# Kernel optimization log

Hardware: AMD Instinct MI355X
Metric: run time of the kernel (lower is better)

Reference implementation:

```python
import jax, jax.numpy as jnp
import numpy as np

N = 4096
F_IN = 128
N_HEADS = 4
N_HIDDEN = 16  # out_features 64 // 4 heads
LRELU_SLOPE = 0.2


def setup_inputs() -> dict:
    key = jax.random.key(0)
    k1, k2, k3 = jax.random.split(key, 3)
    x = jax.random.normal(k1, (N, F_IN), dtype=jnp.float32)
    adj = jax.random.randint(jax.random.fold_in(key, 7), (N, N), 0, 2, dtype=jnp.int32)
    # linearinput weight: in_features -> n_heads * n_hidden (no bias)
    W = jax.random.normal(k2, (F_IN, N_HEADS * N_HIDDEN), dtype=jnp.float32) / np.sqrt(F_IN)
    # attn weight: 2*n_hidden -> 1 (no bias), shared across heads
    attn_w = jax.random.normal(k3, (2 * N_HIDDEN,), dtype=jnp.float32) / np.sqrt(2 * N_HIDDEN)
    return {"x": x, "adj": adj, "W": W, "attn_w": attn_w}


def reference(x, adj, W, attn_w):
    n = x.shape[0]
    # h: (N, H, Dh)
    h = (x @ W).reshape(n, N_HEADS, N_HIDDEN)
    # attn is linear on [h_i || h_j] => e_ij = lrelu(src_i + dst_j)
    a_src = attn_w[:N_HIDDEN]
    a_dst = attn_w[N_HIDDEN:]
    src = jnp.einsum('nhd,d->nh', h, a_src)  # (N, H)
    dst = jnp.einsum('nhd,d->nh', h, a_dst)  # (N, H)
    e = jax.nn.leaky_relu(src[:, None, :] + dst[None, :, :], negative_slope=LRELU_SLOPE)  # (N, N, H)
    a = jax.nn.softmax(e, axis=1)  # softmax over neighbor axis j
    # dropout in eval mode: identity
    attn_res = jnp.einsum('ijh,jhf->ihf', a, h)  # (N, H, Dh)
    return attn_res.reshape(n, N_HEADS * N_HIDDEN)  # is_concat=True
```

## Files before the change

kernel.cpp:

```cpp
#include <hip/hip_runtime.h>

#define NN 4096
#define FIN 128
#define NHEAD 4
#define NHID 16
#define NCOL 64
#define SLOPE 0.2f
#define CHUNK 64
#define NCH 64
#define NCOLS 17
#define RPAD 20

__device__ __forceinline__ float lrelu(float v){ return v > 0.f ? v : SLOPE * v; }

__device__ __forceinline__ unsigned fkey(float f){
  unsigned b = __float_as_uint(f);
  return b ^ ((b & 0x80000000u) ? 0xFFFFFFFFu : 0x80000000u);
}
__device__ __forceinline__ float fkey_inv(unsigned k){
  unsigned b = (k & 0x80000000u) ? (k ^ 0x80000000u) : ~k;
  return __uint_as_float(b);
}

__global__ __launch_bounds__(256) void gemm_h_k(const float* __restrict__ x,
                                                const float* __restrict__ W,
                                                const float* __restrict__ aw,
                                                float* __restrict__ h,
                                                float* __restrict__ src,
                                                float* __restrict__ dst){
  __shared__ __align__(16) float wl[FIN][NCOL];
  __shared__ float xlT[FIN][10];
  __shared__ float hs[8][NCOL + 1];
  int t = threadIdx.x;
  int row0 = blockIdx.x * 8;
  for (int k4 = t; k4 < FIN * NCOL / 4; k4 += 256)
    ((float4*)&wl[0][0])[k4] = ((const float4*)W)[k4];
  for (int k = t; k < 8 * FIN; k += 256){
    int r = k >> 7, d = k & 127;
    xlT[d][r] = x[(row0 + r) * FIN + d];
  }
  __syncthreads();
  int col = t & 63, rb = t >> 6;
  float a0 = 0.f, a1 = 0.f;
  #pragma unroll
  for (int d = 0; d < FIN; ++d){
    float wv = wl[d][col];
    float2 xv = *(const float2*)&xlT[d][rb * 2];
    a0 = fmaf(xv.x, wv, a0);
    a1 = fmaf(xv.y, wv, a1);
  }
  h[(row0 + rb * 2) * NCOL + col] = a0;     hs[rb * 2][col] = a0;
  h[(row0 + rb * 2 + 1) * NCOL + col] = a1; hs[rb * 2 + 1][col] = a1;
  __syncthreads();
  if (t < 32){
    int r = t >> 2, hd = t & 3;
    float s = 0.f, d = 0.f;
    #pragma unroll
    for (int f = 0; f < NHID; ++f){
      float v = hs[r][hd * NHID + f];
      s = fmaf(v, aw[f], s);
      d = fmaf(v, aw[NHID + f], d);
    }
    src[hd * NN + row0 + r] = s;
    dst[hd * NN + row0 + r] = d;
  }
}

__global__ __launch_bounds__(512) void ranksc_k(const float* __restrict__ dst,
                                                unsigned long long* __restrict__ ksort,
                                                unsigned* __restrict__ dkey){
  int ib = blockIdx.x;
  int hd = blockIdx.y;
  __shared__ __align__(16) unsigned long long keys2[64][66];
  __shared__ int wsum[8][64];
  int t = threadIdx.x;
  const float* dp = dst + hd * NN;
  for (int j = t; j < NN; j += 512)
    keys2[j >> 6][j & 63] = ((unsigned long long)fkey(dp[j]) << 32) | (unsigned)j;
  __syncthreads();
  int g = t >> 3, c = t & 7;
  unsigned long long mk[8];
  #pragma unroll
  for (int r = 0; r < 8; ++r) mk[r] = keys2[ib][c * 8 + r];
  int cnt[8] = {0, 0, 0, 0, 0, 0, 0, 0};
  const ulonglong2* kp = (const ulonglong2*)&keys2[g][0];
  #pragma unroll 4
  for (int q = 0; q < 32; ++q){
    ulonglong2 kk = kp[q];
    #pragma unroll
    for (int r = 0; r < 8; ++r){
      cnt[r] += (kk.x < mk[r]) ? 1 : 0;
      cnt[r] += (kk.y < mk[r]) ? 1 : 0;
    }
  }
  #pragma unroll
  for (int r = 0; r < 8; ++r){
    cnt[r] += __shfl_down(cnt[r], 32);
    cnt[r] += __shfl_down(cnt[r], 16);
    cnt[r] += __shfl_down(cnt[r], 8);
  }
  int w = t >> 6;
  if ((t & 63) < 8){
    #pragma unroll
    for (int r = 0; r < 8; ++r) wsum[w][c * 8 + r] = cnt[r];
  }
  __syncthreads();
  if (t < 64){
    int rank = 0;
    #pragma unroll
    for (int w2 = 0; w2 < 8; ++w2) rank += wsum[w2][t];
    unsigned long long key = keys2[ib][t];
    ksort[hd * NN + rank] = key;
    dkey[hd * NN + rank]  = (unsigned)(key >> 32);
  }
}

__global__ __launch_bounds__(256) void scanA_k(const float* __restrict__ h,
                                               const unsigned long long* __restrict__ ksort,
                                               float* __restrict__ PL2,
                                               float* __restrict__ SL2,
                                               float* __restrict__ ctP,
                                               float* __restrict__ ctS){
  int ch = blockIdx.x;
  int hd = blockIdx.y;
  int t = threadIdx.x;
  int base = ch * CHUNK;
  __shared__ float e02[CHUNK], e1[CHUNK];
  __shared__ int   pms[CHUNK];
  __shared__ float hl[CHUNK][RPAD];
  __shared__ float PLs[CHUNK][RPAD], SLs[CHUNK][RPAD];
  if (t < CHUNK){
    unsigned long long key = ksort[hd * NN + base + t];
    float d = fkey_inv((unsigned)(key >> 32));
    e02[t] = __expf(0.2f * d);
    e1[t]  = __expf(d);
    pms[t] = (int)(unsigned)key;
    hl[t][16] = 1.0f;
  }
  __syncthreads();
  {
    int col = t & 15, r0 = t >> 4;
    #pragma unroll
    for (int it = 0; it < 4; ++it){
      int r = it * 16 + r0;
      hl[r][col] = h[pms[r] * NCOL + hd * NHID + col];
    }
  }
  __syncthreads();
  if (t < NCOLS){
    int col = t;
    float run = 0.f;
    #pragma unroll
    for (int r = 0; r < CHUNK; ++r){
      PLs[r][col] = run;
      run = fmaf(e02[r], hl[r][col], run);
    }
    ctP[ch * 68 + hd * 17 + col] = run;
  } else if (t >= 64 && t < 64 + NCOLS){
    int col = t - 64;
    float rs = 0.f;
    #pragma unroll
    for (int r = CHUNK - 1; r >= 0; --r){
      rs = fmaf(e1[r], hl[r][col], rs);
      SLs[r][col] = rs;
    }
    ctS[ch * 68 + hd * 17 + col] = rs;
  }
  __syncthreads();
  #pragma unroll
  for (int n = 0; n < 5; ++n){
    int idx = n * 256 + t;
    int r = idx / RPAD, c = idx % RPAD;
    PL2[(hd * NN + base + r) * RPAD + c] = PLs[r][c];
    SL2[(hd * NN + base + r) * RPAD + c] = SLs[r][c];
  }
}

__global__ __launch_bounds__(256) void out_k(const float* __restrict__ src,
                                             const unsigned* __restrict__ dkey,
                                             const float* __restrict__ PL2,
                                             const float* __restrict__ SL2,
                                             const float* __restrict__ ctP,
                                             const float* __restrict__ ctS,
                                             float* __restrict__ out){
  __shared__ __align__(16) unsigned dk[NN];
  __shared__ __align__(16) float oP[NCH + 1][68];
  __shared__ __align__(16) float oS[NCH][68];
  int t = threadIdx.x;
  int hd = blockIdx.x & 3, ig = blockIdx.x >> 2;
  const unsigned* dkp = dkey + hd * NN;
  #pragma unroll
  for (int n = 0; n < 4; ++n)
    ((uint4*)dk)[n * 256 + t] = ((const uint4*)dkp)[n * 256 + t];
  #pragma unroll
  for (int n = 0; n < 5; ++n){
    int idx = n * 256 + t;
    if (idx < 1088){
      ((float4*)&oP[0][0])[idx] = ((const float4*)ctP)[idx];
      ((float4*)&oS[0][0])[idx] = ((const float4*)ctS)[idx];
    }
  }
  __syncthreads();
  if (t < 68){
    float run = 0.f;
    #pragma unroll
    for (int c = 0; c < NCH; ++c){ float v = oP[c][t]; oP[c][t] = run; run += v; }
    oP[NCH][t] = run;
  } else if (t >= 128 && t < 196){
    int cc = t - 128;
    float rs = 0.f;
    #pragma unroll
    for (int c = NCH - 1; c >= 0; --c){ float v = oS[c][cc]; oS[c][cc] = rs; rs += v; }
  }
  __syncthreads();
  int p = t >> 2, q = t & 3;
  int i = ig * 64 + p;
  float s = src[hd * NN + i];
  unsigned tu = fkey(-s);
  int lo = 0, hi = NN;
  while (lo < hi){
    int mid = (lo + hi) >> 1;
    if (dk[mid] < tu) lo = mid + 1; else hi = mid;
  }
  int k = lo;
  float4 res;
  if (k == NN){
    float inv = 1.0f / oP[NCH][hd * 17 + 16];
    res.x = oP[NCH][hd * 17 + q * 4 + 0] * inv;
    res.y = oP[NCH][hd * 17 + q * 4 + 1] * inv;
    res.z = oP[NCH][hd * 17 + q * 4 + 2] * inv;
    res.w = oP[NCH][hd * 17 + q * 4 + 3] * inv;
  } else {
    float dmax = fkey_inv(dk[NN - 1]);
    float m = lrelu(s + dmax);
    float alpha = __expf(0.2f * s - m);
    float beta  = __expf(s - m);
    int ch = k >> 6;
    const float* P2 = PL2 + (size_t)(hd * NN + k) * RPAD;
    const float* S2 = SL2 + (size_t)(hd * NN + k) * RPAD;
    float4 p4 = *(const float4*)(P2 + q * 4);
    float4 s4 = *(const float4*)(S2 + q * 4);
    float den = alpha * (P2[16] + oP[ch][hd * 17 + 16])
              + beta  * (S2[16] + oS[ch][hd * 17 + 16]);
    float inv = 1.0f / den;
    res.x = (alpha * (p4.x + oP[ch][hd * 17 + q * 4 + 0])
           + beta  * (s4.x + oS[ch][hd * 17 + q * 4 + 0])) * inv;
    res.y = (alpha * (p4.y + oP[ch][hd * 17 + q * 4 + 1])
           + beta  * (s4.y + oS[ch][hd * 17 + q * 4 + 1])) * inv;
    res.z = (alpha * (p4.z + oP[ch][hd * 17 + q * 4 + 2])
           + beta  * (s4.z + oS[ch][hd * 17 + q * 4 + 2])) * inv;
    res.w = (alpha * (p4.w + oP[ch][hd * 17 + q * 4 + 3])
           + beta  * (s4.w + oS[ch][hd * 17 + q * 4 + 3])) * inv;
  }
  *(float4*)(out + i * NCOL + hd * NHID + q * 4) = res;
}

extern "C" void kernel_launch(void* const* d_in, const int* in_sizes, int n_in,
                              void* d_out, int out_size, void* d_ws, size_t ws_size,
                              hipStream_t stream){
  const float* x  = (const float*)d_in[0];
  const float* W  = (const float*)d_in[2];
  const float* aw = (const float*)d_in[3];
  float* out = (float*)d_out;
  float* ws  = (float*)d_ws;

  float*              h     = ws;
  float*              src   = ws + 262144;
  float*              dst   = ws + 278528;
  unsigned long long* ksort = (unsigned long long*)(ws + 294912);
  unsigned*           dkey  = (unsigned*)(ws + 327680);
  float*              PL2   = ws + 344064;
  float*              SL2   = ws + 671744;
  float*              ctP   = ws + 999424;
  float*              ctS   = ws + 1003776;

  gemm_h_k<<<512, 256, 0, stream>>>(x, W, aw, h, src, dst);
  ranksc_k<<<dim3(64, NHEAD), 512, 0, stream>>>(dst, ksort, dkey);
  scanA_k<<<dim3(NCH, NHEAD), 256, 0, stream>>>(h, ksort, PL2, SL2, ctP, ctS);
  out_k<<<256, 256, 0, stream>>>(src, dkey, PL2, SL2, ctP, ctS, out);
}
```

Before: 28.55 us.

## Fuse chunk scan into output kernel, recomputing chunk totals per block

Removes the separate scan kernel and its global prefix/suffix arrays. Each output block loads all sorted keys for its head, recomputes per-chunk weighted sums of h, scans them in shared memory, and finishes each row by accumulating its partial chunk directly. This saves a launch and the PL2/SL2 global traffic. In exchange every block redoes the full per-head chunk reduction with gathered h loads, and each row does a variable-length partial-chunk loop. e1 is derived as e02^5 instead of a second exp.

```diff
diff --git a/kernel.cpp b/kernel.cpp
--- a/kernel.cpp
+++ b/kernel.cpp
@@ -6,10 +6,7 @@
 #define NHID 16
 #define NCOL 64
 #define SLOPE 0.2f
-#define CHUNK 64
 #define NCH 64
-#define NCOLS 17
-#define RPAD 20
 
 __device__ __forceinline__ float lrelu(float v){ return v > 0.f ? v : SLOPE * v; }
 
@@ -21,6 +18,7 @@
   unsigned b = (k & 0x80000000u) ? (k ^ 0x80000000u) : ~k;
   return __uint_as_float(b);
 }
+__device__ __forceinline__ int pidx(int r){ return (r >> 6) * 65 + (r & 63); }
 
 __global__ __launch_bounds__(256) void gemm_h_k(const float* __restrict__ x,
                                                 const float* __restrict__ W,
@@ -67,8 +65,7 @@
 }
 
 __global__ __launch_bounds__(512) void ranksc_k(const float* __restrict__ dst,
-                                                unsigned long long* __restrict__ ksort,
-                                                unsigned* __restrict__ dkey){
+                                                unsigned long long* __restrict__ ksort){
   int ib = blockIdx.x;
   int hd = blockIdx.y;
   __shared__ __align__(16) unsigned long long keys2[64][66];
@@ -109,150 +106,113 @@
     int rank = 0;
     #pragma unroll
     for (int w2 = 0; w2 < 8; ++w2) rank += wsum[w2][t];
-    unsigned long long key = keys2[ib][t];
-    ksort[hd * NN + rank] = key;
-    dkey[hd * NN + rank]  = (unsigned)(key >> 32);
-  }
-}
-
-__global__ __launch_bounds__(256) void scanA_k(const float* __restrict__ h,
-                                               const unsigned long long* __restrict__ ksort,
-                                               float* __restrict__ PL2,
-                                               float* __restrict__ SL2,
-                                               float* __restrict__ ctP,
-                                               float* __restrict__ ctS){
-  int ch = blockIdx.x;
-  int hd = blockIdx.y;
+    ksort[hd * NN + rank] = keys2[ib][t];
+  }
+}
+
+__global__ __launch_bounds__(256) void scanout_k(const float* __restrict__ h,
+                                                 const float* __restrict__ src,
+                                                 const unsigned long long* __restrict__ ksort,
+                                                 float* __restrict__ out){
+  __shared__ __align__(16) unsigned long long dk[NCH * 65];
+  __shared__ float e02p[NCH * 65];
+  __shared__ float ctP[NCH + 1][20], ctS[NCH + 1][20];
   int t = threadIdx.x;
-  int base = ch * CHUNK;
-  __shared__ float e02[CHUNK], e1[CHUNK];
-  __shared__ int   pms[CHUNK];
-  __shared__ float hl[CHUNK][RPAD];
-  __shared__ float PLs[CHUNK][RPAD], SLs[CHUNK][RPAD];
-  if (t < CHUNK){
-    unsigned long long key = ksort[hd * NN + base + t];
-    float d = fkey_inv((unsigned)(key >> 32));
-    e02[t] = __expf(0.2f * d);
-    e1[t]  = __expf(d);
-    pms[t] = (int)(unsigned)key;
-    hl[t][16] = 1.0f;
-  }
-  __syncthreads();
+  int hd = blockIdx.x & 3, ig = blockIdx.x >> 2;
+  const unsigned long long* kp = ksort + hd * NN;
+
+  for (int j = t; j < NN; j += 256) dk[pidx(j)] = kp[j];
+  __syncthreads();
+  for (int j = t; j < NN; j += 256){
+    int pi = pidx(j);
+    e02p[pi] = __expf(0.2f * fkey_inv((unsigned)(dk[pi] >> 32)));
+  }
+  __syncthreads();
+
   {
-    int col = t & 15, r0 = t >> 4;
-    #pragma unroll
-    for (int it = 0; it < 4; ++it){
-      int r = it * 16 + r0;
-      hl[r][col] = h[pms[r] * NCOL + hd * NHID + col];
-    }
-  }
-  __syncthreads();
-  if (t < NCOLS){
-    int col = t;
+    int ch = t >> 2, q = t & 3;
+    float4 aP = {0.f, 0.f, 0.f, 0.f}, aS = {0.f, 0.f, 0.f, 0.f};
+    float dP = 0.f, dS = 0.f;
+    int base = ch * 65;
+    #pragma unroll 4
+    for (int rr = 0; rr < 64; ++rr){
+      unsigned long long key = dk[base + rr];
+      float e  = e02p[base + rr];
+      float p2 = e * e, p4 = p2 * p2;
+      float e1 = p4 * e;
+      const float4 hv = *(const float4*)(h + (size_t)(unsigned)key * NCOL + hd * NHID + q * 4);
+      aP.x = fmaf(e, hv.x, aP.x);  aP.y = fmaf(e, hv.y, aP.y);
+      aP.z = fmaf(e, hv.z, aP.z);  aP.w = fmaf(e, hv.w, aP.w);
+      aS.x = fmaf(e1, hv.x, aS.x); aS.y = fmaf(e1, hv.y, aS.y);
+      aS.z = fmaf(e1, hv.z, aS.z); aS.w = fmaf(e1, hv.w, aS.w);
+      dP += e; dS += e1;
+    }
+    *(float4*)&ctP[ch][q * 4] = aP;
+    *(float4*)&ctS[ch][q * 4] = aS;
+    if (q == 3){ ctP[ch][16] = dP; ctS[ch][16] = dS; }
+  }
+  __syncthreads();
+
+  if (t < 17){
     float run = 0.f;
     #pragma unroll
-    for (int r = 0; r < CHUNK; ++r){
-      PLs[r][col] = run;
-      run = fmaf(e02[r], hl[r][col], run);
-    }
-    ctP[ch * 68 + hd * 17 + col] = run;
-  } else if (t >= 64 && t < 64 + NCOLS){
+    for (int c = 0; c < NCH; ++c){ float v = ctP[c][t]; ctP[c][t] = run; run += v; }
+    ctP[NCH][t] = run;
+  } else if (t >= 64 && t < 81){
     int col = t - 64;
     float rs = 0.f;
     #pragma unroll
-    for (int r = CHUNK - 1; r >= 0; --r){
-      rs = fmaf(e1[r], hl[r][col], rs);
-      SLs[r][col] = rs;
-    }
-    ctS[ch * 68 + hd * 17 + col] = rs;
-  }
-  __syncthreads();
-  #pragma unroll
-  for (int n = 0; n < 5; ++n){
-    int idx = n * 256 + t;
-    int r = idx / RPAD, c = idx % RPAD;
-    PL2[(hd * NN + base + r) * RPAD + c] = PLs[r][c];
-    SL2[(hd * NN + base + r) * RPAD + c] = SLs[r][c];
-  }
-}
-
-__global__ __launch_bounds__(256) void out_k(const float* __restrict__ src,
-                                             const unsigned* __restrict__ dkey,
-                                             const float* __restrict__ PL2,
-                                             const float* __restrict__ SL2,
-                                             const float* __restrict__ ctP,
-                                             const float* __restrict__ ctS,
-                                             float* __restrict__ out){
-  __shared__ __align__(16) unsigned dk[NN];
-  __shared__ __align__(16) float oP[NCH + 1][68];
-  __shared__ __align__(16) float oS[NCH][68];
-  int t = threadIdx.x;
-  int hd = blockIdx.x & 3, ig = blockIdx.x >> 2;
-  const unsigned* dkp = dkey + hd * NN;
-  #pragma unroll
-  for (int n = 0; n < 4; ++n)
-    ((uint4*)dk)[n * 256 + t] = ((const uint4*)dkp)[n * 256 + t];
-  #pragma unroll
-  for (int n = 0; n < 5; ++n){
-    int idx = n * 256 + t;
-    if (idx < 1088){
-      ((float4*)&oP[0][0])[idx] = ((const float4*)ctP)[idx];
-      ((float4*)&oS[0][0])[idx] = ((const float4*)ctS)[idx];
-    }
-  }
-  __syncthreads();
-  if (t < 68){
-    float run = 0.f;
-    #pragma unroll
-    for (int c = 0; c < NCH; ++c){ float v = oP[c][t]; oP[c][t] = run; run += v; }
-    oP[NCH][t] = run;
-  } else if (t >= 128 && t < 196){
-    int cc = t - 128;
-    float rs = 0.f;
-    #pragma unroll
-    for (int c = NCH - 1; c >= 0; --c){ float v = oS[c][cc]; oS[c][cc] = rs; rs += v; }
-  }
-  __syncthreads();
-  int p = t >> 2, q = t & 3;
-  int i = ig * 64 + p;
-  float s = src[hd * NN + i];
-  unsigned tu = fkey(-s);
-  int lo = 0, hi = NN;
-  while (lo < hi){
-    int mid = (lo + hi) >> 1;
-    if (dk[mid] < tu) lo = mid + 1; else hi = mid;
-  }
-  int k = lo;
-  float4 res;
-  if (k == NN){
-    float inv = 1.0f / oP[NCH][hd * 17 + 16];
-    res.x = oP[NCH][hd * 17 + q * 4 + 0] * inv;
-    res.y = oP[NCH][hd * 17 + q * 4 + 1] * inv;
-    res.z = oP[NCH][hd * 17 + q * 4 + 2] * inv;
-    res.w = oP[NCH][hd * 17 + q * 4 + 3] * inv;
-  } else {
-    float dmax = fkey_inv(dk[NN - 1]);
+    for (int c = NCH - 1; c >= 0; --c){ float v = ctS[c][col]; ctS[c][col] = rs; rs += v; }
+    ctS[NCH][col] = 0.f;
+  }
+  __syncthreads();
+
+  {
+    int pr = t >> 2, q = t & 3;
+    int i = ig * 64 + pr;
+    float s = src[hd * NN + i];
+    unsigned long long kk = ((unsigned long long)fkey(-s)) << 32;
+    int lo = 0, hi = NN;
+    while (lo < hi){
+      int mid = (lo + hi) >> 1;
+      if (dk[pidx(mid)] < kk) lo = mid + 1; else hi = mid;
+    }
+    int k = lo;
+    int ch = k >> 6;
+    float4 aP = {0.f, 0.f, 0.f, 0.f}, aS = {0.f, 0.f, 0.f, 0.f};
+    float dP = 0.f, dS = 0.f;
+    for (int r = ch * 64; r < k; ++r){
+      int pi = pidx(r);
+      float e = e02p[pi];
+      const float4 hv = *(const float4*)(h + (size_t)(unsigned)dk[pi] * NCOL + hd * NHID + q * 4);
+      aP.x = fmaf(e, hv.x, aP.x);  aP.y = fmaf(e, hv.y, aP.y);
+      aP.z = fmaf(e, hv.z, aP.z);  aP.w = fmaf(e, hv.w, aP.w);
+      dP += e;
+    }
+    int rend = (ch + 1) * 64; if (rend > NN) rend = NN;
+    for (int r = k; r < rend; ++r){
+      int pi = pidx(r);
+      float e = e02p[pi];
+      float p2 = e * e, p4 = p2 * p2;
+      float e1 = p4 * e;
+      const float4 hv = *(const float4*)(h + (size_t)(unsigned)dk[pi] * NCOL + hd * NHID + q * 4);
+      aS.x = fmaf(e1, hv.x, aS.x); aS.y = fmaf(e1, hv.y, aS.y);
+      aS.z = fmaf(e1, hv.z, aS.z); aS.w = fmaf(e1, hv.w, aS.w);
+      dS += e1;
+    }
+    float dmax = fkey_inv((unsigned)(dk[pidx(NN - 1)] >> 32));
     float m = lrelu(s + dmax);
     float alpha = __expf(0.2f * s - m);
     float beta  = __expf(s - m);
-    int ch = k >> 6;
-    const float* P2 = PL2 + (size_t)(hd * NN + k) * RPAD;
-    const float* S2 = SL2 + (size_t)(hd * NN + k) * RPAD;
-    float4 p4 = *(const float4*)(P2 + q * 4);
-    float4 s4 = *(const float4*)(S2 + q * 4);
-    float den = alpha * (P2[16] + oP[ch][hd * 17 + 16])
-              + beta  * (S2[16] + oS[ch][hd * 17 + 16]);
+    float den = alpha * (ctP[ch][16] + dP) + beta * (ctS[ch][16] + dS);
     float inv = 1.0f / den;
-    res.x = (alpha * (p4.x + oP[ch][hd * 17 + q * 4 + 0])
-           + beta  * (s4.x + oS[ch][hd * 17 + q * 4 + 0])) * inv;
-    res.y = (alpha * (p4.y + oP[ch][hd * 17 + q * 4 + 1])
-           + beta  * (s4.y + oS[ch][hd * 17 + q * 4 + 1])) * inv;
-    res.z = (alpha * (p4.z + oP[ch][hd * 17 + q * 4 + 2])
-           + beta  * (s4.z + oS[ch][hd * 17 + q * 4 + 2])) * inv;
-    res.w = (alpha * (p4.w + oP[ch][hd * 17 + q * 4 + 3])
-           + beta  * (s4.w + oS[ch][hd * 17 + q * 4 + 3])) * inv;
-  }
-  *(float4*)(out + i * NCOL + hd * NHID + q * 4) = res;
+    float4 res;
+    res.x = (alpha * (ctP[ch][q * 4 + 0] + aP.x) + beta * (ctS[ch][q * 4 + 0] + aS.x)) * inv;
+    res.y = (alpha * (ctP[ch][q * 4 + 1] + aP.y) + beta * (ctS[ch][q * 4 + 1] + aS.y)) * inv;
+    res.z = (alpha * (ctP[ch][q * 4 + 2] + aP.z) + beta * (ctS[ch][q * 4 + 2] + aS.z)) * inv;
+    res.w = (alpha * (ctP[ch][q * 4 + 3] + aP.w) + beta * (ctS[ch][q * 4 + 3] + aS.w)) * inv;
+    *(float4*)(out + (size_t)i * NCOL + hd * NHID + q * 4) = res;
+  }
 }
 
 extern "C" void kernel_launch(void* const* d_in, const int* in_sizes, int n_in,
@@ -268,14 +228,8 @@
   float*              src   = ws + 262144;
   float*              dst   = ws + 278528;
   unsigned long long* ksort = (unsigned long long*)(ws + 294912);
-  unsigned*           dkey  = (unsigned*)(ws + 327680);
-  float*              PL2   = ws + 344064;
-  float*              SL2   = ws + 671744;
-  float*              ctP   = ws + 999424;
-  float*              ctS   = ws + 1003776;
 
   gemm_h_k<<<512, 256, 0, stream>>>(x, W, aw, h, src, dst);
-  ranksc_k<<<dim3(64, NHEAD), 512, 0, stream>>>(dst, ksort, dkey);
-  scanA_k<<<dim3(NCH, NHEAD), 256, 0, stream>>>(h, ksort, PL2, SL2, ctP, ctS);
-  out_k<<<256, 256, 0, stream>>>(src, dkey, PL2, SL2, ctP, ctS, out);
-}
+  ranksc_k<<<dim3(64, NHEAD), 512, 0, stream>>>(dst, ksort);
+  scanout_k<<<256, 256, 0, stream>>>(h, src, ksort, out);
+}
```

New measurement: 54.03 us. +89.2%, slower.
